# Kernel optimization log

Measured on AMD Instinct MI355X. Metric: run time of the kernel, lower is better.

Reference implementation:

```python
import jax, jax.numpy as jnp
from jax import lax
import numpy as np

COST_CLASS, COST_BBOX, COST_GIOU = 2.0, 5.0, 2.0
ALPHA, GAMMA, OTA_K = 0.25, 2.0, 5
EXPANDED_STRIDES = 32.0
DEG = 180.0 / np.pi


def _make_corners(key, prefix):
    k1, k2, k3, k4, k5 = jax.random.split(key, 5)
    cx = jax.random.uniform(k1, prefix, minval=0.0, maxval=512.0)
    cy = jax.random.uniform(k2, prefix, minval=0.0, maxval=512.0)
    w = jax.random.uniform(k3, prefix, minval=8.0, maxval=128.0)
    h = jax.random.uniform(k4, prefix, minval=8.0, maxval=128.0)
    ang = jax.random.uniform(k5, prefix, minval=0.0, maxval=np.pi)
    offs = jnp.array([[-0.5, -0.5], [0.5, -0.5], [0.5, 0.5], [-0.5, 0.5]], jnp.float32)
    wh = jnp.stack([w, h], -1)[..., None, :]          # [..., 1, 2]
    pts = offs * wh                                    # [..., 4, 2]
    c, s = jnp.cos(ang)[..., None], jnp.sin(ang)[..., None]
    rx = pts[..., 0] * c - pts[..., 1] * s + cx[..., None]
    ry = pts[..., 0] * s + pts[..., 1] * c + cy[..., None]
    return jnp.stack([rx, ry], -1).reshape(prefix + (8,))


def setup_inputs() -> dict:
    key = jax.random.key(0)
    k1, k2, k3, k4 = jax.random.split(key, 4)
    B, Q, G, C = 16, 4096, 128, 80
    return {
        "pred_logits": jax.random.normal(k1, (B, Q, C), jnp.float32),
        "pred_boxes": _make_corners(k2, (B, Q)),
        "gt_boxes": _make_corners(k3, (B, G)),
        "gt_labels": jax.random.randint(k4, (B, G), 0, C),
    }


def corners_to_cxcywha(c):  # [N,8] -> [N,5]
    xc = (c[:, 0] + c[:, 2] + c[:, 4] + c[:, 6]) / 4
    yc = (c[:, 1] + c[:, 3] + c[:, 5] + c[:, 7]) / 4
    w = jnp.sqrt((c[:, 0] - c[:, 2]) ** 2 + (c[:, 1] - c[:, 3]) ** 2)
    h = jnp.sqrt((c[:, 2] - c[:, 4]) ** 2 + (c[:, 3] - c[:, 5]) ** 2)
    ang = jnp.arctan2(c[:, 3] - c[:, 1], c[:, 2] - c[:, 0]) * DEG
    return jnp.stack([xc, yc, w, h, ang], 1)


def _aabb(b5):
    cx, cy, w, h = b5[:, 0], b5[:, 1], b5[:, 2], b5[:, 3]
    return jnp.stack([cx - w / 2, cy - h / 2, cx + w / 2, cy + h / 2], 1)


def pairwise_iou(b1, b2):
    a, b = _aabb(b1), _aabb(b2)
    lt = jnp.maximum(a[:, None, :2], b[None, :, :2])
    rb = jnp.minimum(a[:, None, 2:], b[None, :, 2:])
    wh = jnp.clip(rb - lt, 0.0)
    inter = wh[..., 0] * wh[..., 1]
    area1 = (a[:, 2] - a[:, 0]) * (a[:, 3] - a[:, 1])
    area2 = (b[:, 2] - b[:, 0]) * (b[:, 3] - b[:, 1])
    return inter / (area1[:, None] + area2[None, :] - inter + 1e-8)


def pairwise_diou(b1, b2):
    iou = pairwise_iou(b1, b2)
    a, b = _aabb(b1), _aabb(b2)
    enc = jnp.maximum(a[:, None, 2:], b[None, :, 2:]) - jnp.minimum(a[:, None, :2], b[None, :, :2])
    c2 = (enc ** 2).sum(-1) + 1e-8
    d2 = ((b1[:, None, :2] - b2[None, :, :2]) ** 2).sum(-1)
    return iou - d2 / c2


def get_in_boxes_info(boxes, gts):
    bc = boxes.reshape(-1, 4, 2).mean(1)   # [Q,2]
    gp = gts.reshape(-1, 4, 2)             # [G,4,2]
    gc = gp.mean(1)                        # [G,2]
    cdist = jnp.sqrt(((bc[:, None] - gc[None]) ** 2).sum(-1))  # [Q,G]
    v1 = gp[:, 1] - gp[:, 0]
    v2 = gp[:, 2] - gp[:, 0]
    gt_area = jnp.abs(v1[:, 0] * v2[:, 1] - v1[:, 1] * v2[:, 0]) / 2
    diag = jnp.sqrt(((gp.max(1) - gp.min(1)) ** 2).sum(-1))
    radius = diag / EXPANDED_STRIDES
    in_boxes = cdist <= (gt_area / radius)[None, :]
    in_centers = cdist <= radius[None, :]
    return in_boxes.any(1), in_boxes & in_centers


def _dedup(cost, m):
    multi = m.sum(1) > 1
    onehot = jax.nn.one_hot(jnp.argmin(cost, 1), cost.shape[1], dtype=m.dtype)
    return jnp.where(multi[:, None], onehot, m)


def _match_single(logits, pboxes, gboxes, glabels):
    Q, G = pboxes.shape[0], gboxes.shape[0]
    prob = jax.nn.sigmoid(logits)
    fg_mask, _ = get_in_boxes_info(pboxes, gboxes)
    p5, g5 = corners_to_cxcywha(pboxes), corners_to_cxcywha(gboxes)
    ious = pairwise_iou(p5, g5)
    neg = (1 - ALPHA) * prob ** GAMMA * -jnp.log(1 - prob + 1e-8)
    pos = ALPHA * (1 - prob) ** GAMMA * -jnp.log(prob + 1e-8)
    cost_class = (pos - neg)[:, glabels]                         # [Q,G]
    cost_bbox = jnp.abs(pboxes[:, None] - gboxes[None]).sum(-1)  # L1 cdist on corners
    cost_giou = -pairwise_diou(p5, g5)
    # NB: source has `+ self.cost_giou * -cost_giou`, i.e. +w*diou; replicated verbatim.
    cost = COST_BBOX * cost_bbox + COST_CLASS * cost_class + COST_GIOU * (-cost_giou)
    cost = cost + 10000.0 * (~fg_mask)[:, None].astype(cost.dtype)
    # dynamic-k: sum of top OTA_K ious per gt, truncated to int, min 1
    topk = lax.top_k(ious.T, OTA_K)[0]                 # [G, k]
    dyn_k = jnp.clip(topk.sum(-1).astype(jnp.int32), 1, Q)
    ranks = jnp.argsort(jnp.argsort(cost, axis=0), axis=0)  # ascending-cost rank per column
    matching = (ranks < dyn_k[None, :]).astype(cost.dtype)
    matching = _dedup(cost, matching)
    # ensure every gt matched (bounded replication of the while loop)
    def cond(carry):
        c, m, it = carry
        return jnp.any(m.sum(0) == 0) & (it < G)
    def body(carry):
        c, m, it = carry
        c = c + 100000.0 * (m.sum(1) > 0)[:, None].astype(c.dtype)
        unm = m.sum(0) == 0
        amin = jnp.argmin(c, 0)                          # [G]
        hit = (jnp.arange(Q)[:, None] == amin[None, :]) & unm[None, :]
        m = jnp.where(hit, 1.0, m)
        m = _dedup(c, m)
        return (c, m, it + 1)
    _, matching, _ = lax.while_loop(cond, body, (cost, matching, jnp.int32(0)))
    return matching, cost, ious


def reference(pred_logits, pred_boxes, gt_boxes, gt_labels):
    return jax.vmap(_match_single)(pred_logits, pred_boxes, gt_boxes, gt_labels)
```

## Files before the change

### kernel.cpp

```cpp
#include <hip/hip_runtime.h>
#include <cstdint>
#include <cstddef>

#define B_ 16
#define Q_ 4096
#define G_ 128
#define C_ 80
#define QCHUNK 16
#define NCH (Q_ / QCHUNK)

typedef unsigned long long u64;
#define U64MAX 0xffffffffffffffffull

__device__ __forceinline__ u64 packkey(float v, int q) {
    unsigned int bts = __float_as_uint(v);
    if (bts == 0x80000000u) bts = 0u;
    bts = (bts & 0x80000000u) ? ~bts : (bts | 0x80000000u);
    return ((u64)bts << 32) | (unsigned int)q;
}

__device__ __forceinline__ u64 umin64(u64 a, u64 b) { return a < b ? a : b; }
__device__ __forceinline__ u64 umax64(u64 a, u64 b) { return a > b ? a : b; }

__device__ __forceinline__ void merge5_desc(
    float& a0, float& a1, float& a2, float& a3, float& a4,
    float b0, float b1, float b2, float b3, float b4)
{
    const float r0 = fmaxf(a0, b0);
    const float r1 = fmaxf(fmaxf(a1, b1), fminf(a0, b0));
    const float r2 = fmaxf(fmaxf(a2, b2), fmaxf(fminf(a0, b1), fminf(a1, b0)));
    const float r3 = fmaxf(fmaxf(a3, b3),
                     fmaxf(fminf(a0, b2), fmaxf(fminf(a1, b1), fminf(a2, b0))));
    const float r4 = fmaxf(fmaxf(a4, b4),
                     fmaxf(fmaxf(fminf(a0, b3), fminf(a3, b0)),
                           fmaxf(fminf(a1, b2), fminf(a2, b1))));
    a0 = r0; a1 = r1; a2 = r2; a3 = r3; a4 = r4;
}

__device__ __forceinline__ void merge5_asc(
    u64& a0, u64& a1, u64& a2, u64& a3, u64& a4,
    u64 b0, u64 b1, u64 b2, u64 b3, u64 b4)
{
    const u64 r0 = umin64(a0, b0);
    const u64 r1 = umin64(umin64(a1, b1), umax64(a0, b0));
    const u64 r2 = umin64(umin64(a2, b2), umin64(umax64(a0, b1), umax64(a1, b0)));
    const u64 r3 = umin64(umin64(a3, b3),
                   umin64(umax64(a0, b2), umin64(umax64(a1, b1), umax64(a2, b0))));
    const u64 r4 = umin64(umin64(a4, b4),
                   umin64(umin64(umax64(a0, b3), umax64(a3, b0)),
                          umin64(umax64(a1, b2), umax64(a2, b1))));
    a0 = r0; a1 = r1; a2 = r2; a3 = r3; a4 = r4;
}

__device__ __forceinline__ float focal_cost(float x) {
    float p;
    if (x >= 0.f) { const float e = expf(-x); p = 1.f / (1.f + e); }
    else          { const float e = expf(x);  p = e / (1.f + e); }
    const float pos = 0.25f * (1.f - p) * (1.f - p) * (-logf(p + 1e-8f));
    const float neg = 0.75f * p * p * (-logf(1.f - p + 1e-8f));
    return pos - neg;
}

__global__ __launch_bounds__(256) void fused_cost_kernel(
    const float* __restrict__ logits,
    const float* __restrict__ pboxes,
    const float* __restrict__ gboxes,
    const int*   __restrict__ glabels,
    float* __restrict__ out_cost,
    float* __restrict__ out_iou,
    float* __restrict__ piou,
    u64*   __restrict__ pcost,
    int*   __restrict__ ramin,
    int*   __restrict__ cnt)
{
    const int tid = threadIdx.x;
    const int g   = tid & 127;
    const int qh  = tid >> 7;
    const int ci  = blockIdx.x, b = blockIdx.y;
    const int q0  = ci * QCHUNK;

    __shared__ float pq[QCHUNK][16];
    __shared__ int   fgf[QCHUNK];
    __shared__ __align__(16) char lk_buf[5120];
    __shared__ float ctile[QCHUNK][G_ + 1];
    __shared__ float phalf[G_][5];
    float* lbuf = (float*)lk_buf;
    u64 (*khalf)[5] = (u64(*)[5])lk_buf;

    if (tid < QCHUNK) cnt[b * Q_ + q0 + tid] = 0;

    const float4* gb4 = (const float4*)(gboxes + ((size_t)b * G_ + g) * 8);
    const float4 gA = gb4[0], gB = gb4[1];
    const float g0 = gA.x, g1 = gA.y, g2 = gA.z, g3 = gA.w;
    const float g4 = gB.x, g5 = gB.y, g6 = gB.z, g7 = gB.w;
    const float gxc = (g0 + g2 + g4 + g6) * 0.25f;
    const float gyc = (g1 + g3 + g5 + g7) * 0.25f;
    const float gw = sqrtf((g0 - g2) * (g0 - g2) + (g1 - g3) * (g1 - g3));
    const float gh = sqrtf((g2 - g4) * (g2 - g4) + (g3 - g5) * (g3 - g5));
    const float gax0 = gxc - gw * 0.5f, gay0 = gyc - gh * 0.5f;
    const float gax1 = gxc + gw * 0.5f, gay1 = gyc + gh * 0.5f;
    const float garea = (gax1 - gax0) * (gay1 - gay0);
    const float v1x = g2 - g0, v1y = g3 - g1, v2x = g4 - g0, v2y = g5 - g1;
    const float gt_area = fabsf(v1x * v2y - v1y * v2x) * 0.5f;
    const float mxx = fmaxf(fmaxf(g0, g2), fmaxf(g4, g6));
    const float mnx = fminf(fminf(g0, g2), fminf(g4, g6));
    const float mxy = fmaxf(fmaxf(g1, g3), fmaxf(g5, g7));
    const float mny = fminf(fminf(g1, g3), fminf(g5, g7));
    const float dgx = mxx - mnx, dgy = mxy - mny;
    const float radius = sqrtf(dgx * dgx + dgy * dgy) / 32.0f;
    const float thresh = gt_area / radius;
    const int lab = glabels[b * G_ + g];

    if (tid < 32) {
        const float4 v = ((const float4*)(pboxes + ((size_t)b * Q_ + q0) * 8))[tid];
        *(float4*)&pq[tid >> 1][(tid & 1) * 4] = v;
    }
    __syncthreads();
    if (tid < QCHUNK) {
        const float* pr = pq[tid];
        const float p0 = pr[0], p1 = pr[1], p2 = pr[2], p3 = pr[3];
        const float p4 = pr[4], p5v = pr[5], p6 = pr[6], p7 = pr[7];
        const float pxc = (p0 + p2 + p4 + p6) * 0.25f;
        const float pyc = (p1 + p3 + p5v + p7) * 0.25f;
        const float pw = sqrtf((p0 - p2) * (p0 - p2) + (p1 - p3) * (p1 - p3));
        const float ph = sqrtf((p2 - p4) * (p2 - p4) + (p3 - p5v) * (p3 - p5v));
        pq[tid][8]  = pxc;
        pq[tid][9]  = pyc;
        pq[tid][10] = pxc - pw * 0.5f;
        pq[tid][11] = pyc - ph * 0.5f;
        pq[tid][12] = pxc + pw * 0.5f;
        pq[tid][13] = pyc + ph * 0.5f;
        pq[tid][14] = pw * ph;
        fgf[tid] = 0;
    }
    __syncthreads();
    for (int j = tid; j < QCHUNK * 80; j += 256)
        lbuf[j] = focal_cost(logits[((size_t)b * Q_ + q0) * 80 + j]);

    const int lane0 = ((tid & 63) == 0);
    for (int i = 0; i < QCHUNK / 2; ++i) {
        const int ql = 2 * i + qh;
        const float dx = pq[ql][8] - gxc, dy = pq[ql][9] - gyc;
        const int in = sqrtf(dx * dx + dy * dy) <= thresh;
        const int anyin = __any(in);
        if (anyin && lane0) fgf[ql] = 1;
    }
    __syncthreads();

    float t0 = -1e38f, t1 = -1e38f, t2 = -1e38f, t3 = -1e38f, t4 = -1e38f;
    u64 k0 = U64MAX, k1 = U64MAX, k2 = U64MAX, k3 = U64MAX, k4 = U64MAX;

    #pragma unroll
    for (int jj = 0; jj < 8; ++jj) {
        const int qls = 2 * jj + qh;
        const int q   = q0 + qls;
        const float4 prA = *(const float4*)&pq[qls][0];
        const float4 prB = *(const float4*)&pq[qls][4];
        const float4 prC = *(const float4*)&pq[qls][8];
        const float4 prD = *(const float4*)&pq[qls][12];
        const float p0 = prA.x, p1 = prA.y, p2 = prA.z, p3 = prA.w;
        const float p4 = prB.x, p5v = prB.y, p6 = prB.z, p7 = prB.w;
        const float pxc = prC.x, pyc = prC.y;
        const float pax0 = prC.z, pay0 = prC.w, pax1 = prD.x, pay1 = prD.y;
        const float parea = prD.z;

        const float l1 = fabsf(p0 - g0) + fabsf(p1 - g1) + fabsf(p2 - g2)
                       + fabsf(p3 - g3) + fabsf(p4 - g4) + fabsf(p5v - g5)
                       + fabsf(p6 - g6) + fabsf(p7 - g7);

        const float ltx = fmaxf(pax0, gax0), lty = fmaxf(pay0, gay0);
        const float rbx = fminf(pax1, gax1), rby = fminf(pay1, gay1);
        const float iw = fmaxf(rbx - ltx, 0.f), ih = fmaxf(rby - lty, 0.f);
        const float inter = iw * ih;
        const float iou = inter / (parea + garea - inter + 1e-8f);

        const float ew = fmaxf(pax1, gax1) - fminf(pax0, gax0);
        const float eh = fmaxf(pay1, gay1) - fminf(pay0, gay0);
        const float cc2 = ew * ew + eh * eh + 1e-8f;
        const float dx = pxc - gxc, dy = pyc - gyc;
        const float diou = iou - (dx * dx + dy * dy) / cc2;

        const float cclass = lbuf[qls * 80 + lab];
        const float cost = 5.f * l1 + 2.f * cclass + 2.f * diou
                         + (fgf[qls] ? 0.f : 10000.f);

        const size_t o = ((size_t)b * Q_ + q) * G_ + g;
        out_cost[o] = cost;
        out_iou[o]  = iou;
        ctile[qls][g] = cost;

        if (iou > t4) {
            if (iou > t0)      { t4 = t3; t3 = t2; t2 = t1; t1 = t0; t0 = iou; }
            else if (iou > t1) { t4 = t3; t3 = t2; t2 = t1; t1 = iou; }
            else if (iou > t2) { t4 = t3; t3 = t2; t2 = iou; }
            else if (iou > t3) { t4 = t3; t3 = iou; }
            else               { t4 = iou; }
        }
        const u64 kk = packkey(cost, q);
        if (kk < k4) {
            if (kk < k0)      { k4 = k3; k3 = k2; k2 = k1; k1 = k0; k0 = kk; }
            else if (kk < k1) { k4 = k3; k3 = k2; k2 = k1; k1 = kk; }
            else if (kk < k2) { k4 = k3; k3 = k2; k2 = kk; }
            else if (kk < k3) { k4 = k3; k3 = kk; }
            else              { k4 = kk; }
        }
    }
    __syncthreads();

    {
        const int qls  = tid >> 4;
        const int part = tid & 15;
        float v = 1e38f; int mg = 0x7fffffff;
        #pragma unroll
        for (int j = 0; j < 8; ++j) {
            const int gg = part + 16 * j;
            const float c = ctile[qls][gg];
            if (c < v || (c == v && gg < mg)) { v = c; mg = gg; }
        }
        #pragma unroll
        for (int off = 1; off < 16; off <<= 1) {
            const float ov = __shfl_xor(v, off);
            const int   og = __shfl_xor(mg, off);
            if (ov < v || (ov == v && og < mg)) { v = ov; mg = og; }
        }
        if (part == 0) ramin[b * Q_ + q0 + qls] = mg;
    }

    if (qh == 1) {
        phalf[g][0] = t0; phalf[g][1] = t1; phalf[g][2] = t2;
        phalf[g][3] = t3; phalf[g][4] = t4;
        khalf[g][0] = k0; khalf[g][1] = k1; khalf[g][2] = k2;
        khalf[g][3] = k3; khalf[g][4] = k4;
    }
    __syncthreads();
    if (qh == 0) {
        merge5_desc(t0, t1, t2, t3, t4,
                    phalf[g][0], phalf[g][1], phalf[g][2], phalf[g][3], phalf[g][4]);
        merge5_asc(k0, k1, k2, k3, k4,
                   khalf[g][0], khalf[g][1], khalf[g][2], khalf[g][3], khalf[g][4]);
        const size_t pbase = (((size_t)b * NCH + ci) * G_ + g) * 5;
        piou[pbase + 0] = t0; piou[pbase + 1] = t1; piou[pbase + 2] = t2;
        piou[pbase + 3] = t3; piou[pbase + 4] = t4;
        pcost[pbase + 0] = k0; pcost[pbase + 1] = k1; pcost[pbase + 2] = k2;
        pcost[pbase + 3] = k3; pcost[pbase + 4] = k4;
    }
}

__global__ __launch_bounds__(256) void dynk_scatter_kernel(
    const u64*   __restrict__ pcost,
    const float* __restrict__ piou,
    u64* __restrict__ cand,
    int* __restrict__ cnt,
    int* __restrict__ gsel)
{
    const int col = blockIdx.x;
    const int b = col >> 7, g = col & 127;
    const int tid = threadIdx.x;
    const int wv = tid >> 6, ln = tid & 63;

    __shared__ u64   wl[4][5];
    __shared__ float il[4][5];

    const size_t base = (((size_t)b * NCH + tid) * G_ + g) * 5;

    u64 k0 = pcost[base + 0], k1 = pcost[base + 1], k2 = pcost[base + 2],
        k3 = pcost[base + 3], k4 = pcost[base + 4];
    float t0 = piou[base + 0], t1 = piou[base + 1], t2 = piou[base + 2],
          t3 = piou[base + 3], t4 = piou[base + 4];

    #pragma unroll
    for (int off = 1; off < 64; off <<= 1) {
        merge5_asc(k0, k1, k2, k3, k4,
                   __shfl_xor(k0, off), __shfl_xor(k1, off), __shfl_xor(k2, off),
                   __shfl_xor(k3, off), __shfl_xor(k4, off));
        merge5_desc(t0, t1, t2, t3, t4,
                    __shfl_xor(t0, off), __shfl_xor(t1, off), __shfl_xor(t2, off),
                    __shfl_xor(t3, off), __shfl_xor(t4, off));
    }
    if (ln == 0) {
        wl[wv][0] = k0; wl[wv][1] = k1; wl[wv][2] = k2; wl[wv][3] = k3; wl[wv][4] = k4;
        il[wv][0] = t0; il[wv][1] = t1; il[wv][2] = t2; il[wv][3] = t3; il[wv][4] = t4;
    }
    __syncthreads();

    if (tid == 0) {
        u64 f0 = wl[0][0], f1 = wl[0][1], f2 = wl[0][2], f3 = wl[0][3], f4 = wl[0][4];
        merge5_asc(f0, f1, f2, f3, f4, wl[1][0], wl[1][1], wl[1][2], wl[1][3], wl[1][4]);
        merge5_asc(f0, f1, f2, f3, f4, wl[2][0], wl[2][1], wl[2][2], wl[2][3], wl[2][4]);
        merge5_asc(f0, f1, f2, f3, f4, wl[3][0], wl[3][1], wl[3][2], wl[3][3], wl[3][4]);
        float s0 = il[0][0], s1 = il[0][1], s2 = il[0][2], s3 = il[0][3], s4 = il[0][4];
        merge5_desc(s0, s1, s2, s3, s4, il[1][0], il[1][1], il[1][2], il[1][3], il[1][4]);
        merge5_desc(s0, s1, s2, s3, s4, il[2][0], il[2][1], il[2][2], il[2][3], il[2][4]);
        merge5_desc(s0, s1, s2, s3, s4, il[3][0], il[3][1], il[3][2], il[3][3], il[3][4]);

        cand[(size_t)col * 5 + 0] = f0;
        cand[(size_t)col * 5 + 1] = f1;
        cand[(size_t)col * 5 + 2] = f2;
        cand[(size_t)col * 5 + 3] = f3;
        cand[(size_t)col * 5 + 4] = f4;

        const float s = s0 + s1 + s2 + s3 + s4;
        int dynk = (int)s;
        if (dynk < 1) dynk = 1;
        if (dynk > 5) dynk = 5;
        const u64 ks[5] = {f0, f1, f2, f3, f4};
        #pragma unroll
        for (int i = 0; i < 5; ++i) {
            if (i < dynk) {
                const int q = (int)(ks[i] & 0xffffffffu);
                atomicAdd(&cnt[b * Q_ + q], 1);
                gsel[b * Q_ + q] = g;
            }
        }
    }
}

__global__ __launch_bounds__(1024) void loop_kernel(
    const float* __restrict__ cost,
    const int* __restrict__ cnt,
    const int* __restrict__ gsel,
    const int* __restrict__ ramin,
    const u64* __restrict__ cand,
    int* __restrict__ rmatch_final)
{
    const int b = blockIdx.x, tid = threadIdx.x;
    const int wv = tid >> 6, ln = tid & 63;

    __shared__ short rmatch[Q_];
    __shared__ unsigned char s_ra[Q_];
    __shared__ int newh[Q_];
    __shared__ unsigned char newg[Q_];
    __shared__ u64 scand[G_][5];
    __shared__ int ptrs[G_], col_cnt[G_], unm_list[G_], prop[G_], fb_slot[G_], touched[G_];
    __shared__ int n_unm, n_fb, n_touch;

    for (int q = tid; q < Q_; q += 1024) {
        const int c  = cnt[b * Q_ + q];
        const int ra = ramin[b * Q_ + q];
        s_ra[q] = (unsigned char)ra;
        newh[q] = 0;
        rmatch[q] = (c == 0) ? (short)-1
                             : (c == 1 ? (short)gsel[b * Q_ + q] : (short)ra);
    }
    if (tid < G_) { col_cnt[tid] = 0; ptrs[tid] = 0; }
    if (tid < G_ * 5)
        scand[tid / 5][tid % 5] = cand[(size_t)b * G_ * 5 + tid];
    __syncthreads();
    for (int q = tid; q < Q_; q += 1024)
        if (rmatch[q] >= 0) atomicAdd(&col_cnt[rmatch[q]], 1);
    __syncthreads();

    const float* costb = cost + (size_t)b * Q_ * G_;

    for (int it = 0; it < G_; ++it) {
        if (tid == 0) { n_unm = 0; n_fb = 0; n_touch = 0; }
        __syncthreads();
        if (tid < G_ && col_cnt[tid] == 0)
            unm_list[atomicAdd(&n_unm, 1)] = tid;
        __syncthreads();
        const int nu = n_unm;
        if (nu == 0) break;

        if (tid < nu) {
            const int g = unm_list[tid];
            int p = ptrs[g];
            int q = -1;
            while (p < 5) {
                const int cq = (int)(scand[g][p] & 0xffffffffu);
                if (rmatch[cq] < 0) { q = cq; break; }
                ++p;
            }
            ptrs[g] = p;
            prop[tid] = q;
            if (q < 0) fb_slot[atomicAdd(&n_fb, 1)] = tid;
        }
        __syncthreads();

        const int nf = n_fb;
        for (int i = wv; i < nf; i += 16) {
            const int slot = fb_slot[i];
            const int g = unm_list[slot];
            const float* colp = costb + g;
            u64 k0 = U64MAX, k1 = U64MAX, k2 = U64MAX, k3 = U64MAX, k4 = U64MAX;
            for (int q = ln; q < Q_; q += 64) {
                if (rmatch[q] < 0) {
                    const float v = colp[(size_t)q * G_];
                    const u64 kk = packkey(v, q);
                    if (kk < k4) {
                        if (kk < k0)      { k4 = k3; k3 = k2; k2 = k1; k1 = k0; k0 = kk; }
                        else if (kk < k1) { k4 = k3; k3 = k2; k2 = k1; k1 = kk; }
                        else if (kk < k2) { k4 = k3; k3 = k2; k2 = kk; }
                        else if (kk < k3) { k4 = k3; k3 = kk; }
                        else              { k4 = kk; }
                    }
                }
            }
            #pragma unroll
            for (int off = 1; off < 64; off <<= 1) {
                merge5_asc(k0, k1, k2, k3, k4,
                           __shfl_xor(k0, off), __shfl_xor(k1, off), __shfl_xor(k2, off),
                           __shfl_xor(k3, off), __shfl_xor(k4, off));
            }
            if (ln == 0) {
                scand[g][0] = k0; scand[g][1] = k1; scand[g][2] = k2;
                scand[g][3] = k3; scand[g][4] = k4;
                ptrs[g] = 0;
                prop[slot] = (int)(k0 & 0xffffffffu);
            }
        }
        __syncthreads();

        if (tid < nu) {
            const int q = prop[tid];
            newg[q] = (unsigned char)unm_list[tid];
            if (atomicAdd(&newh[q], 1) == 0)
                touched[atomicAdd(&n_touch, 1)] = q;
        }
        __syncthreads();

        const int nt = n_touch;
        if (tid < nt) {
            const int q = touched[tid];
            const int nh = newh[q];
            const int gg = (nh == 1) ? (int)newg[q] : (int)s_ra[q];
            rmatch[q] = (short)gg;
            atomicAdd(&col_cnt[gg], 1);
            newh[q] = 0;
        }
        __syncthreads();
    }

    for (int q = tid; q < Q_; q += 1024)
        rmatch_final[b * Q_ + q] = rmatch[q];
}

__global__ __launch_bounds__(256) void expand_kernel(
    const int* __restrict__ rmatch_final, float* __restrict__ out_match)
{
    const int idx = blockIdx.x * 256 + threadIdx.x;
    const int row = idx >> 5;
    const int gb  = (idx & 31) << 2;
    const int rm  = rmatch_final[row];
    float4 o;
    o.x = (rm == gb)     ? 1.f : 0.f;
    o.y = (rm == gb + 1) ? 1.f : 0.f;
    o.z = (rm == gb + 2) ? 1.f : 0.f;
    o.w = (rm == gb + 3) ? 1.f : 0.f;
    ((float4*)out_match)[idx] = o;
}

extern "C" void kernel_launch(void* const* d_in, const int* in_sizes, int n_in,
                              void* d_out, int out_size, void* d_ws, size_t ws_size,
                              hipStream_t stream) {
    const float* logits  = (const float*)d_in[0];
    const float* pboxes  = (const float*)d_in[1];
    const float* gboxes  = (const float*)d_in[2];
    const int*   glabels = (const int*)d_in[3];

    float* out = (float*)d_out;
    const size_t BQG = (size_t)B_ * Q_ * G_;
    float* out_match = out;
    float* out_cost  = out + BQG;
    float* out_iou   = out + 2 * BQG;

    char* ws = (char*)d_ws;
    size_t off = 0;
    u64*   pcost  = (u64*)  (ws + off); off += (size_t)B_ * NCH * G_ * 5 * 8;
    float* piou   = (float*)(ws + off); off += (size_t)B_ * NCH * G_ * 5 * 4;
    u64*   cand   = (u64*)  (ws + off); off += (size_t)B_ * G_ * 5 * 8;
    int*   ramin  = (int*)  (ws + off); off += (size_t)B_ * Q_ * 4;
    int*   cnt    = (int*)  (ws + off); off += (size_t)B_ * Q_ * 4;
    int*   gsel   = (int*)  (ws + off); off += (size_t)B_ * Q_ * 4;
    int*   rmf    = (int*)  (ws + off); off += (size_t)B_ * Q_ * 4;

    fused_cost_kernel<<<dim3(NCH, B_), 256, 0, stream>>>(
        logits, pboxes, gboxes, glabels, out_cost, out_iou, piou, pcost, ramin, cnt);
    dynk_scatter_kernel<<<B_ * G_, 256, 0, stream>>>(pcost, piou, cand, cnt, gsel);
    loop_kernel<<<B_, 1024, 0, stream>>>(out_cost, cnt, gsel, ramin, cand, rmf);
    expand_kernel<<<(int)(BQG / 4 / 256), 256, 0, stream>>>(rmf, out_match);
}
```

Measured before the change: 197.0 us.

## Restructure per-chunk top-5 selection into branchless column scans over shared tile

Instead of each thread keeping branchy running top-5 lists for cost and IoU across its half of the chunk and then merging the halves through shared memory, the kernel now writes (cost, iou) pairs into a shared tile. Threads 0-127 then do a branchless insertion-network scan over all 16 rows per gt column, while threads 128-255 at the same time compute the per-row argmin. This removes warp divergence, the 64-bit key comparisons and one barrier-plus-merge phase. In exchange it adds a serial 16-step scan on half the threads and uses more shared memory. Tie handling in the argmin now relies on a strict less-than scan order plus the index tiebreak in the shuffle reduction.

```diff
diff --git a/kernel.cpp b/kernel.cpp
--- a/kernel.cpp
+++ b/kernel.cpp
@@ -59,6 +59,15 @@
     const float pos = 0.25f * (1.f - p) * (1.f - p) * (-logf(p + 1e-8f));
     const float neg = 0.75f * p * p * (-logf(1.f - p + 1e-8f));
     return pos - neg;
+}
+
+__device__ __forceinline__ void ins_level(float& c, int& j, float& x, int& qx) {
+    const bool s  = x < c;
+    const float nc = s ? x : c;
+    const float nx = s ? c : x;
+    const int   nj = s ? qx : j;
+    const int   nq = s ? j : qx;
+    c = nc; x = nx; j = nj; qx = nq;
 }
 
 __global__ __launch_bounds__(256) void fused_cost_kernel(
@@ -81,11 +90,8 @@
 
     __shared__ float pq[QCHUNK][16];
     __shared__ int   fgf[QCHUNK];
-    __shared__ __align__(16) char lk_buf[5120];
-    __shared__ float ctile[QCHUNK][G_ + 1];
-    __shared__ float phalf[G_][5];
-    float* lbuf = (float*)lk_buf;
-    u64 (*khalf)[5] = (u64(*)[5])lk_buf;
+    __shared__ float lbuf[QCHUNK * 80];
+    __shared__ float2 citile[QCHUNK][G_ + 2];
 
     if (tid < QCHUNK) cnt[b * Q_ + q0 + tid] = 0;
 
@@ -147,9 +153,6 @@
     }
     __syncthreads();
 
-    float t0 = -1e38f, t1 = -1e38f, t2 = -1e38f, t3 = -1e38f, t4 = -1e38f;
-    u64 k0 = U64MAX, k1 = U64MAX, k2 = U64MAX, k3 = U64MAX, k4 = U64MAX;
-
     #pragma unroll
     for (int jj = 0; jj < 8; ++jj) {
         const int qls = 2 * jj + qh;
@@ -187,62 +190,56 @@
         const size_t o = ((size_t)b * Q_ + q) * G_ + g;
         out_cost[o] = cost;
         out_iou[o]  = iou;
-        ctile[qls][g] = cost;
-
-        if (iou > t4) {
-            if (iou > t0)      { t4 = t3; t3 = t2; t2 = t1; t1 = t0; t0 = iou; }
-            else if (iou > t1) { t4 = t3; t3 = t2; t2 = t1; t1 = iou; }
-            else if (iou > t2) { t4 = t3; t3 = t2; t2 = iou; }
-            else if (iou > t3) { t4 = t3; t3 = iou; }
-            else               { t4 = iou; }
-        }
-        const u64 kk = packkey(cost, q);
-        if (kk < k4) {
-            if (kk < k0)      { k4 = k3; k3 = k2; k2 = k1; k1 = k0; k0 = kk; }
-            else if (kk < k1) { k4 = k3; k3 = k2; k2 = k1; k1 = kk; }
-            else if (kk < k2) { k4 = k3; k3 = k2; k2 = kk; }
-            else if (kk < k3) { k4 = k3; k3 = kk; }
-            else              { k4 = kk; }
-        }
-    }
-    __syncthreads();
-
-    {
-        const int qls  = tid >> 4;
-        const int part = tid & 15;
+        citile[qls][g] = make_float2(cost, iou);
+    }
+    __syncthreads();
+
+    if (tid < G_) {
+        float c0 = 1e38f, c1 = 1e38f, c2 = 1e38f, c3 = 1e38f, c4 = 1e38f;
+        int   j0 = 0, j1 = 0, j2 = 0, j3 = 0, j4 = 0;
+        float t0 = 0.f, t1 = 0.f, t2 = 0.f, t3 = 0.f, t4 = 0.f;
+        #pragma unroll
+        for (int q = 0; q < QCHUNK; ++q) {
+            const float2 cv = citile[q][tid];
+            float x = cv.x; int qx = q;
+            ins_level(c0, j0, x, qx);
+            ins_level(c1, j1, x, qx);
+            ins_level(c2, j2, x, qx);
+            ins_level(c3, j3, x, qx);
+            ins_level(c4, j4, x, qx);
+            float y = cv.y, m;
+            m = fmaxf(t0, y); y = fminf(t0, y); t0 = m;
+            m = fmaxf(t1, y); y = fminf(t1, y); t1 = m;
+            m = fmaxf(t2, y); y = fminf(t2, y); t2 = m;
+            m = fmaxf(t3, y); y = fminf(t3, y); t3 = m;
+            t4 = fmaxf(t4, y);
+        }
+        const size_t pbase = (((size_t)b * NCH + ci) * G_ + tid) * 5;
+        piou[pbase + 0] = t0; piou[pbase + 1] = t1; piou[pbase + 2] = t2;
+        piou[pbase + 3] = t3; piou[pbase + 4] = t4;
+        pcost[pbase + 0] = packkey(c0, q0 + j0);
+        pcost[pbase + 1] = packkey(c1, q0 + j1);
+        pcost[pbase + 2] = packkey(c2, q0 + j2);
+        pcost[pbase + 3] = packkey(c3, q0 + j3);
+        pcost[pbase + 4] = packkey(c4, q0 + j4);
+    } else {
+        const int t    = tid - 128;
+        const int part = t & 7;
+        const int row  = t >> 3;
         float v = 1e38f; int mg = 0x7fffffff;
         #pragma unroll
-        for (int j = 0; j < 8; ++j) {
-            const int gg = part + 16 * j;
-            const float c = ctile[qls][gg];
-            if (c < v || (c == v && gg < mg)) { v = c; mg = gg; }
+        for (int j = 0; j < 16; ++j) {
+            const int gg = part + 8 * j;
+            const float c = citile[row][gg].x;
+            if (c < v) { v = c; mg = gg; }
         }
         #pragma unroll
-        for (int off = 1; off < 16; off <<= 1) {
+        for (int off = 1; off < 8; off <<= 1) {
             const float ov = __shfl_xor(v, off);
             const int   og = __shfl_xor(mg, off);
             if (ov < v || (ov == v && og < mg)) { v = ov; mg = og; }
         }
-        if (part == 0) ramin[b * Q_ + q0 + qls] = mg;
-    }
-
-    if (qh == 1) {
-        phalf[g][0] = t0; phalf[g][1] = t1; phalf[g][2] = t2;
-        phalf[g][3] = t3; phalf[g][4] = t4;
-        khalf[g][0] = k0; khalf[g][1] = k1; khalf[g][2] = k2;
-        khalf[g][3] = k3; khalf[g][4] = k4;
-    }
-    __syncthreads();
-    if (qh == 0) {
-        merge5_desc(t0, t1, t2, t3, t4,
-                    phalf[g][0], phalf[g][1], phalf[g][2], phalf[g][3], phalf[g][4]);
-        merge5_asc(k0, k1, k2, k3, k4,
-                   khalf[g][0], khalf[g][1], khalf[g][2], khalf[g][3], khalf[g][4]);
-        const size_t pbase = (((size_t)b * NCH + ci) * G_ + g) * 5;
-        piou[pbase + 0] = t0; piou[pbase + 1] = t1; piou[pbase + 2] = t2;
-        piou[pbase + 3] = t3; piou[pbase + 4] = t4;
-        pcost[pbase + 0] = k0; pcost[pbase + 1] = k1; pcost[pbase + 2] = k2;
-        pcost[pbase + 3] = k3; pcost[pbase + 4] = k4;
+        if (part == 0) ramin[b * Q_ + q0 + row] = mg;
     }
 }
 
```

Result: no change. 196.7 us (-0.1%).
